# Optimization experiments

Measured on AMD Instinct MI355X. Metric: run time of the kernel, lower is better.

Reference implementation:

```python
import jax, jax.numpy as jnp
import numpy as np

B, N, D, H, HID = 8, 512, 512, 8, 2048


def setup_inputs() -> dict:
    key = jax.random.key(0)
    ks = jax.random.split(key, 8)
    s = 0.02
    p = lambda i, shape: jax.random.normal(ks[i], shape, jnp.float32) * s
    return dict(
        x=jax.random.normal(ks[0], (B, N, D), jnp.float32),
        Wq=p(1, (D, D)), bq=jnp.zeros((D,), jnp.float32),
        Wk=p(2, (D, D)), bk=jnp.zeros((D,), jnp.float32),
        Wv=p(3, (D, D)), bv=jnp.zeros((D,), jnp.float32),
        Wsig=p(4, (H, D)), bsig=jnp.zeros((H,), jnp.float32),
        ln1_g=jnp.ones((D,), jnp.float32), ln1_b=jnp.zeros((D,), jnp.float32),
        W1=p(5, (HID, D)), b1=jnp.zeros((HID,), jnp.float32),
        W2=p(6, (D, HID)), b2=jnp.zeros((D,), jnp.float32),
        ln2_g=jnp.ones((D,), jnp.float32), ln2_b=jnp.zeros((D,), jnp.float32),
    )


def _ln(z, g, b, eps=1e-5):
    m = jnp.mean(z, axis=-1, keepdims=True)
    v = jnp.var(z, axis=-1, keepdims=True)
    return (z - m) * jax.lax.rsqrt(v + eps) * g + b


def reference(x, Wq, bq, Wk, bk, Wv, bv, Wsig, bsig,
              ln1_g, ln1_b, W1, b1, W2, b2, ln2_g, ln2_b):
    Bb, Nn, Dd = x.shape
    Hh = bsig.shape[0]
    dh = Dd // Hh
    # --- AnomalyAttention: series attention S, Gaussian prior P, Z = S @ V ---
    Q = (x @ Wq.T + bq).reshape(Bb, Nn, Hh, dh)
    K = (x @ Wk.T + bk).reshape(Bb, Nn, Hh, dh)
    V = (x @ Wv.T + bv).reshape(Bb, Nn, Hh, dh)
    scores = jnp.einsum('bnhd,bmhd->bhnm', Q, K) / jnp.sqrt(jnp.float32(dh))
    S = jax.nn.softmax(scores, axis=-1)                       # [B,H,N,N]
    # learned positive scale sigma per (batch, position, head)
    sigma = jax.nn.softplus(x @ Wsig.T + bsig) + 1e-5         # [B,N,H]
    idx = jnp.arange(Nn, dtype=jnp.float32)
    dist2 = (idx[:, None] - idx[None, :]) ** 2                # [N,N]
    sig = jnp.transpose(sigma, (0, 2, 1))[..., None]          # [B,H,N,1]
    gauss = jnp.exp(-dist2 / (2.0 * sig * sig)) / (jnp.sqrt(2.0 * jnp.pi) * sig)
    P = gauss / jnp.sum(gauss, axis=-1, keepdims=True)        # row-normalized prior
    Zh = jnp.einsum('bhnm,bmhd->bnhd', S, V).reshape(Bb, Nn, Dd)
    # --- residual + LayerNorm + MLP(relu) + residual + LayerNorm ---
    Z = _ln(Zh + x, ln1_g, ln1_b)
    hidden = jax.nn.relu(Z @ W1.T + b1)
    x_hat = hidden @ W2.T + b2
    x_hat = _ln(x_hat + Z, ln2_g, ln2_b)
    return (x_hat, P, S)
```

## Files before the change

kernel.cpp:

```cpp
#include <hip/hip_runtime.h>
#include <cstdint>

typedef short s16x8 __attribute__((ext_vector_type(8)));
typedef float f32x4 __attribute__((ext_vector_type(4)));
using u16 = unsigned short;


__device__ __forceinline__ u16 f2bf(float f) {
    union { float f; uint32_t u; } v; v.f = f;
    uint32_t u = v.u;
    return (u16)((u + 0x7FFFu + ((u >> 16) & 1u)) >> 16);
}
__device__ __forceinline__ float bf2f(u16 u) {
    return __uint_as_float(((uint32_t)u) << 16);
}

__device__ __forceinline__ void gload_lds16(const void* g, void* l) {
    __builtin_amdgcn_global_load_lds(
        (const __attribute__((address_space(1))) unsigned int*)g,
        (__attribute__((address_space(3))) unsigned int*)l, 16, 0, 0);
}

__device__ __forceinline__ void prior_row(
    const float* __restrict__ sigT, float* __restrict__ P, int row, int lane)
{
    int n = row & 511;
    float s = sigT[row];
    float a = -1.0f / (2.0f * s * s);
    float e[8]; float sum = 0.f;
#pragma unroll
    for (int j = 0; j < 8; ++j) {
        float d = (float)(n - (lane * 8 + j));
        e[j] = __expf(a * d * d);
        sum += e[j];
    }
#pragma unroll
    for (int m = 1; m < 64; m <<= 1) sum += __shfl_xor(sum, m, 64);
    float r = 1.0f / sum;
    f32x4* dst = (f32x4*)(P + (long)row * 512 + lane * 8);
    dst[0] = (f32x4){e[0]*r, e[1]*r, e[2]*r, e[3]*r};
    dst[1] = (f32x4){e[4]*r, e[5]*r, e[6]*r, e[7]*r};
}

__global__ __launch_bounds__(256) void k_convert_sigma(
    const float* __restrict__ x, const float* __restrict__ wq,
    const float* __restrict__ wk, const float* __restrict__ wv,
    const float* __restrict__ w1, const float* __restrict__ w2,
    const float* __restrict__ bq, const float* __restrict__ bk,
    const float* __restrict__ bv,
    const float* __restrict__ Wsig, const float* __restrict__ bsig,
    u16* __restrict__ xb, u16* __restrict__ wqb, u16* __restrict__ wkb,
    u16* __restrict__ wvb, u16* __restrict__ w1b, u16* __restrict__ w2b,
    float* __restrict__ biascat, float* __restrict__ sigT)
{
    int bk_ = blockIdx.x;
    int tid = threadIdx.x;
    if (bk_ >= 4866) {
        int row  = (int)(((bk_ - 4866) * 256 + tid) >> 6);
        int lane = tid & 63;
        const float4* xr = (const float4*)(x + (long)row * 512);
        float4 xa = xr[lane * 2], xc = xr[lane * 2 + 1];
        float xs[8] = {xa.x, xa.y, xa.z, xa.w, xc.x, xc.y, xc.z, xc.w};
        float ph[8];
#pragma unroll
        for (int h = 0; h < 8; ++h) {
            const float4* wr = (const float4*)(Wsig + h * 512);
            float4 wa = wr[lane * 2], wc = wr[lane * 2 + 1];
            ph[h] = xs[0]*wa.x + xs[1]*wa.y + xs[2]*wa.z + xs[3]*wa.w
                  + xs[4]*wc.x + xs[5]*wc.y + xs[6]*wc.z + xs[7]*wc.w;
        }
#pragma unroll
        for (int h = 0; h < 8; ++h)
#pragma unroll
            for (int m = 1; m < 64; m <<= 1)
                ph[h] += __shfl_xor(ph[h], m, 64);
        if (lane < 8) {
            float z  = ph[lane] + bsig[lane];
            float sp = fmaxf(z, 0.f) + log1pf(__expf(-fabsf(z)));
            int b = row >> 9, n = row & 511;
            sigT[(((long)b * 8 + lane) << 9) + n] = sp + 1e-5f;
        }
        return;
    }
    long g = (long)bk_ * 256 + tid;
    if (g >= 1245184) {
        long id = g - 1245184;
        if (id < 384) {
            const float* src = id < 128 ? bq : id < 256 ? bk : bv;
            ((float4*)biascat)[id] = ((const float4*)src)[id & 127];
        }
        return;
    }
    const float* src; u16* dst; long off;
    if      (g <  524288) { src = x;  dst = xb;  off = g; }
    else if (g <  589824) { src = wq; dst = wqb; off = g -  524288; }
    else if (g <  655360) { src = wk; dst = wkb; off = g -  589824; }
    else if (g <  720896) { src = wv; dst = wvb; off = g -  655360; }
    else if (g <  983040) { src = w1; dst = w1b; off = g -  720896; }
    else                  { src = w2; dst = w2b; off = g -  983040; }
    float4 v = ((const float4*)src)[off];
    ushort4 o;
    o.x = f2bf(v.x); o.y = f2bf(v.y); o.z = f2bf(v.z); o.w = f2bf(v.w);
    ((ushort4*)dst)[off] = o;
}

template<int EPI>
__device__ __forceinline__ void gemm_epi(
    const float* __restrict__ bias, void* __restrict__ C,
    int gi, int gj, float v)
{
    if constexpr (EPI == 3) {
        v = fmaxf(v + bias[gj], 0.f);
        ((u16*)C)[(long)gi * 2048 + gj] = f2bf(v);
    } else if constexpr (EPI == 4) {
        ((float*)C)[(long)gi * 512 + gj] = v + bias[gj];
    } else {
        v += bias[gj];
        int mat = gj >> 9, cj = gj & 511;
        int h = cj >> 6, d = cj & 63, b = gi >> 9, n = gi & 511;
        u16* base = (u16*)C;
        if (mat == 0)
            base[(((long)(b * 8 + h) * 512 + n) << 6) + d] = f2bf(v);
        else if (mat == 1)
            (base + 2097152)[(((long)(b * 8 + h) * 512 + n) << 6) + d] = f2bf(v);
        else
            (base + 4194304)[(((long)(b * 8 + h) * 64 + d) << 9) + n] = f2bf(v);
    }
}

template<int BM, int BN, int EPI>
__device__ __forceinline__ void gemm_body(
    const u16* __restrict__ A, const u16* __restrict__ B,
    const float* __restrict__ bias, void* __restrict__ C,
    int lda, int ldb, int K, int bx, int by,
    u16* __restrict__ As, u16* __restrict__ Bs)
{
    constexpr int BK = 64;
    const u16* Ag = A + (long)bx * BM * lda;
    const u16* Bg = B + (long)by * BN * ldb;

    int tid  = threadIdx.x;
    int wave = tid >> 6, lane = tid & 63;
    int wm = wave >> 2, wn = wave & 3;
    constexpr int WTM = BM / 2, WTN = BN / 4;
    constexpr int FM = WTM / 16, FN = WTN / 16;
    int r16 = lane & 15, g4 = lane >> 4;

    f32x4 acc[FM][FN];
#pragma unroll
    for (int i = 0; i < FM; ++i)
#pragma unroll
        for (int j = 0; j < FN; ++j) acc[i][j] = (f32x4){0.f, 0.f, 0.f, 0.f};

    constexpr int nA = BM * BK / (512 * 8);
    constexpr int nB = BN * BK / (512 * 8);

    auto stage = [&](int buf, int k0) {
#pragma unroll
        for (int c = 0; c < nA; ++c) {
            int e = c * 512 + tid;
            int r = e >> 3, s = e & 7;
            gload_lds16(Ag + (long)r * lda + k0 + ((s ^ (r & 7)) * 8),
                        &As[buf * BM * BK + e * 8]);
        }
#pragma unroll
        for (int c = 0; c < nB; ++c) {
            int e = c * 512 + tid;
            int r = e >> 3, s = e & 7;
            gload_lds16(Bg + (long)r * ldb + k0 + ((s ^ (r & 7)) * 8),
                        &Bs[buf * BN * BK + e * 8]);
        }
    };

    stage(0, 0);
    __syncthreads();
    int cur = 0;
    const int NT = K / BK;
    for (int t = 0; t < NT; ++t) {
        if (t + 1 < NT) stage(cur ^ 1, (t + 1) * BK);
#pragma unroll
        for (int kk = 0; kk < 2; ++kk) {
            s16x8 af[FM], bfr[FN];
#pragma unroll
            for (int fm = 0; fm < FM; ++fm) {
                int row = wm * WTM + fm * 16 + r16;
                int slot = (kk * 4 + g4) ^ (row & 7);
                af[fm] = *(const s16x8*)&As[cur * BM * BK + row * 64 + slot * 8];
            }
#pragma unroll
            for (int fn = 0; fn < FN; ++fn) {
                int row = wn * WTN + fn * 16 + r16;
                int slot = (kk * 4 + g4) ^ (row & 7);
                bfr[fn] = *(const s16x8*)&Bs[cur * BN * BK + row * 64 + slot * 8];
            }
#pragma unroll
            for (int fm = 0; fm < FM; ++fm)
#pragma unroll
                for (int fn = 0; fn < FN; ++fn)
                    acc[fm][fn] = __builtin_amdgcn_mfma_f32_16x16x32_bf16(af[fm], bfr[fn], acc[fm][fn], 0, 0, 0);
        }
        __syncthreads();
        cur ^= 1;
    }

    int i0 = bx * BM + wm * WTM;
    int j0 = by * BN + wn * WTN;
#pragma unroll
    for (int fm = 0; fm < FM; ++fm)
#pragma unroll
        for (int fn = 0; fn < FN; ++fn)
#pragma unroll
            for (int j = 0; j < 4; ++j)
                gemm_epi<EPI>(bias, C,
                              i0 + fm * 16 + (g4 << 2) + j,
                              j0 + fn * 16 + r16, acc[fm][fn][j]);
}

template<int BM, int BN, int EPI>
__global__ __launch_bounds__(512) void k_gemm_nt(
    const u16* __restrict__ A, const u16* __restrict__ B,
    const float* __restrict__ bias, void* __restrict__ C,
    int lda, int ldb, int K)
{
    __shared__ __align__(16) u16 As[2 * BM * 64];
    __shared__ __align__(16) u16 Bs[2 * BN * 64];
    gemm_body<BM, BN, EPI>(A, B, bias, C, lda, ldb, K,
                           blockIdx.x, blockIdx.y, As, Bs);
}

__global__ __launch_bounds__(512) void k_qkv_prior(
    const u16* __restrict__ A, const u16* __restrict__ B,
    const float* __restrict__ bias, void* __restrict__ C,
    const float* __restrict__ sigT, float* __restrict__ P)
{
    __shared__ __align__(16) u16 As[2 * 128 * 64];
    __shared__ __align__(16) u16 Bs[2 * 128 * 64];
    int gid = blockIdx.x;
    if (gid < 384) {
        gemm_body<128, 128, 5>(A, B, bias, C, 512, 512, 512,
                               gid % 32, gid / 32, As, Bs);
        return;
    }
    int pid  = gid - 384;
    int wave = threadIdx.x >> 6, lane = threadIdx.x & 63;
    prior_row(sigT, P, 16384 + pid * 8 + wave, lane);
}

__global__ __launch_bounds__(256) void k_attn_prior(
    const u16* __restrict__ Qb, const u16* __restrict__ Kb,
    const u16* __restrict__ Vt, const float* __restrict__ sigT,
    float* __restrict__ S, float* __restrict__ Zh, float* __restrict__ P)
{
    __shared__ __align__(16) u16 Sb[4][16][264];
    __shared__ float cmbM[2][2][16];
    __shared__ float cmbS[2][2][16];
    __shared__ float zc[2][16][66];

    int gid = blockIdx.x;
    int tid = threadIdx.x;
    int wave = tid >> 6, lane = tid & 63;

    if (gid >= 1024) {
        prior_row(sigT, P, (gid - 1024) * 4 + wave, lane);
        return;
    }

    int bh = gid & 63;
    int rb = gid >> 6;
    int rg = wave >> 1, ch = wave & 1;
    int r16 = lane & 15, g4 = lane >> 4, hi8 = g4 * 8;

    int row0 = rb * 32 + rg * 16;
    const u16* Qg = Qb + ((long)bh * 512 + row0) * 64;
    const u16* Kg = Kb + ((long)bh * 512 + ch * 256) * 64;
    const u16* Vg = Vt + (long)bh * 64 * 512;

    s16x8 qa[2];
    qa[0] = *(const s16x8*)(Qg + r16 * 64 + hi8);
    qa[1] = *(const s16x8*)(Qg + r16 * 64 + 32 + hi8);

    f32x4 acc[16];
#pragma unroll
    for (int t = 0; t < 16; ++t) acc[t] = (f32x4){0.f, 0.f, 0.f, 0.f};

    __builtin_amdgcn_s_setprio(1);
#pragma unroll
    for (int kk = 0; kk < 2; ++kk)
#pragma unroll
        for (int t = 0; t < 16; ++t) {
            s16x8 b = *(const s16x8*)(Kg + (long)(t * 16 + r16) * 64 + kk * 32 + hi8);
            acc[t] = __builtin_amdgcn_mfma_f32_16x16x32_bf16(qa[kk], b, acc[t], 0, 0, 0);
        }
    __builtin_amdgcn_s_setprio(0);

    float mx[4] = {-1e30f, -1e30f, -1e30f, -1e30f};
#pragma unroll
    for (int t = 0; t < 16; ++t)
#pragma unroll
        for (int j = 0; j < 4; ++j) mx[j] = fmaxf(mx[j], acc[t][j]);
#pragma unroll
    for (int j = 0; j < 4; ++j)
#pragma unroll
        for (int m = 1; m < 16; m <<= 1) mx[j] = fmaxf(mx[j], __shfl_xor(mx[j], m, 64));

    float sm[4] = {0.f, 0.f, 0.f, 0.f};
#pragma unroll
    for (int t = 0; t < 16; ++t)
#pragma unroll
        for (int j = 0; j < 4; ++j) {
            float p = __expf(0.125f * (acc[t][j] - mx[j]));
            acc[t][j] = p;
            sm[j] += p;
        }
#pragma unroll
    for (int j = 0; j < 4; ++j)
#pragma unroll
        for (int m = 1; m < 16; m <<= 1) sm[j] += __shfl_xor(sm[j], m, 64);

    if (r16 == 0) {
#pragma unroll
        for (int j = 0; j < 4; ++j) {
            cmbM[rg][ch][g4 * 4 + j] = mx[j];
            cmbS[rg][ch][g4 * 4 + j] = sm[j];
        }
    }
    __syncthreads();

    float scale[4];
#pragma unroll
    for (int j = 0; j < 4; ++j) {
        float mo = cmbM[rg][ch ^ 1][g4 * 4 + j];
        float so = cmbS[rg][ch ^ 1][g4 * 4 + j];
        float M  = fmaxf(mx[j], mo);
        float tot = sm[j] * __expf(mx[j] - M) + so * __expf(mo - M);
        scale[j] = __expf(mx[j] - M) / tot;
    }
#pragma unroll
    for (int t = 0; t < 16; ++t)
#pragma unroll
        for (int j = 0; j < 4; ++j) acc[t][j] *= scale[j];

#pragma unroll
    for (int t = 0; t < 16; ++t)
#pragma unroll
        for (int j = 0; j < 4; ++j)
            Sb[wave][g4 * 4 + j][t * 16 + r16] = f2bf(acc[t][j]);

    long sbase = ((long)bh * 512 + row0) * 512 + ch * 256;
#pragma unroll
    for (int r = 0; r < 16; ++r) {
        ushort4 u = *(const ushort4*)&Sb[wave][r][lane * 4];
        *(f32x4*)&S[sbase + (long)r * 512 + lane * 4] =
            (f32x4){bf2f(u.x), bf2f(u.y), bf2f(u.z), bf2f(u.w)};
    }

    f32x4 zacc[4];
#pragma unroll
    for (int fn = 0; fn < 4; ++fn) zacc[fn] = (f32x4){0.f, 0.f, 0.f, 0.f};

    __builtin_amdgcn_s_setprio(1);
#pragma unroll
    for (int kb = 0; kb < 8; ++kb) {
        s16x8 pa = *(const s16x8*)&Sb[wave][r16][kb * 32 + hi8];
#pragma unroll
        for (int fn = 0; fn < 4; ++fn) {
            s16x8 vb = *(const s16x8*)(Vg + (long)(fn * 16 + r16) * 512 + ch * 256 + kb * 32 + hi8);
            zacc[fn] = __builtin_amdgcn_mfma_f32_16x16x32_bf16(pa, vb, zacc[fn], 0, 0, 0);
        }
    }
    __builtin_amdgcn_s_setprio(0);

    if (ch == 1) {
#pragma unroll
        for (int fn = 0; fn < 4; ++fn)
#pragma unroll
            for (int j = 0; j < 4; ++j)
                zc[rg][g4 * 4 + j][fn * 16 + r16] = zacc[fn][j];
    }
    __syncthreads();
    if (ch == 0) {
        long zb = ((long)(bh >> 3) * 512 + row0) * 512 + (bh & 7) * 64;
#pragma unroll
        for (int fn = 0; fn < 4; ++fn)
#pragma unroll
            for (int j = 0; j < 4; ++j)
                Zh[zb + (long)(g4 * 4 + j) * 512 + fn * 16 + r16] =
                    zacc[fn][j] + zc[rg][g4 * 4 + j][fn * 16 + r16];
    }
}

template<bool WBF>
__global__ __launch_bounds__(256) void k_ln(
    const float* __restrict__ a, const float* __restrict__ b,
    const float* __restrict__ g, const float* __restrict__ bt,
    float* __restrict__ y, u16* __restrict__ yb)
{
    int row  = (int)((blockIdx.x * 256 + threadIdx.x) >> 6);
    int lane = threadIdx.x & 63;
    const float4* ar = (const float4*)(a + (long)row * 512);
    const float4* br = (const float4*)(b + (long)row * 512);
    float4 a0 = ar[lane * 2], a1 = ar[lane * 2 + 1];
    float4 b0 = br[lane * 2], b1 = br[lane * 2 + 1];
    float v[8] = {a0.x + b0.x, a0.y + b0.y, a0.z + b0.z, a0.w + b0.w,
                  a1.x + b1.x, a1.y + b1.y, a1.z + b1.z, a1.w + b1.w};
    float s = 0.f, q = 0.f;
#pragma unroll
    for (int j = 0; j < 8; ++j) { s += v[j]; q += v[j] * v[j]; }
#pragma unroll
    for (int m = 1; m < 64; m <<= 1) {
        s += __shfl_xor(s, m, 64);
        q += __shfl_xor(q, m, 64);
    }
    float mean = s * (1.f / 512.f);
    float var  = q * (1.f / 512.f) - mean * mean;
    float rstd = rsqrtf(var + 1e-5f);
    const float4* gr = (const float4*)(g + lane * 8);
    const float4* tr = (const float4*)(bt + lane * 8);
    float4 g0 = gr[0], g1 = gr[1], t0 = tr[0], t1 = tr[1];
    float gg[8] = {g0.x, g0.y, g0.z, g0.w, g1.x, g1.y, g1.z, g1.w};
    float tt[8] = {t0.x, t0.y, t0.z, t0.w, t1.x, t1.y, t1.z, t1.w};
    float o[8];
#pragma unroll
    for (int j = 0; j < 8; ++j) o[j] = (v[j] - mean) * rstd * gg[j] + tt[j];
    float4* yr = (float4*)(y + (long)row * 512 + lane * 8);
    yr[0] = make_float4(o[0], o[1], o[2], o[3]);
    yr[1] = make_float4(o[4], o[5], o[6], o[7]);
    if constexpr (WBF) {
        s16x8 ob;
#pragma unroll
        for (int j = 0; j < 8; ++j) ob[j] = (short)f2bf(o[j]);
        *(s16x8*)(yb + (long)row * 512 + lane * 8) = ob;
    }
}

extern "C" void kernel_launch(void* const* d_in, const int* in_sizes, int n_in,
                              void* d_out, int out_size, void* d_ws, size_t ws_size,
                              hipStream_t stream)
{
    const float* x    = (const float*)d_in[0];
    const float* Wq   = (const float*)d_in[1];
    const float* bq   = (const float*)d_in[2];
    const float* Wk   = (const float*)d_in[3];
    const float* bk   = (const float*)d_in[4];
    const float* Wv   = (const float*)d_in[5];
    const float* bv   = (const float*)d_in[6];
    const float* Wsig = (const float*)d_in[7];
    const float* bsig = (const float*)d_in[8];
    const float* g1   = (const float*)d_in[9];
    const float* be1  = (const float*)d_in[10];
    const float* W1   = (const float*)d_in[11];
    const float* b1   = (const float*)d_in[12];
    const float* W2   = (const float*)d_in[13];
    const float* b2   = (const float*)d_in[14];
    const float* g2   = (const float*)d_in[15];
    const float* be2  = (const float*)d_in[16];

    float* out_xhat = (float*)d_out;
    float* out_P    = out_xhat + 2097152;
    float* out_S    = out_P + 16777216;

    char* ws = (char*)d_ws;
    u16*   xb   = (u16*)(ws + 0);
    u16*   Qb   = (u16*)(ws + 4194304);
    u16*   hid  = (u16*)(ws + 0);
    u16*   Wqb  = (u16*)(ws + 16777216);
    u16*   W1b  = (u16*)(ws + 18350080);
    u16*   W2b  = (u16*)(ws + 20447232);
    float* sigT = (float*)(ws + 22544384);
    float* Zh   = (float*)(ws + 22675456);
    float* bcat = (float*)(ws + 22675456);
    float* x2   = (float*)(ws + 22675456);
    float* Z    = (float*)(ws + 31064064);
    u16*   Zb   = (u16*)(ws + 39452672);

    u16* Wkb = Wqb + 262144;
    u16* Wvb = Wqb + 524288;

    k_convert_sigma<<<5890, 256, 0, stream>>>(x, Wq, Wk, Wv, W1, W2, bq, bk, bv,
                                              Wsig, bsig,
                                              xb, Wqb, Wkb, Wvb, W1b, W2b,
                                              bcat, sigT);

    k_qkv_prior<<<2432, 512, 0, stream>>>(xb, Wqb, bcat, Qb, sigT, out_P);

    k_attn_prior<<<5120, 256, 0, stream>>>(Qb, Qb + 2097152, Qb + 4194304,
                                           sigT, out_S, Zh, out_P);

    k_ln<true><<<1024,256,0,stream>>>(Zh, x, g1, be1, Z, Zb);

    k_gemm_nt<128,128,3><<<dim3(32,16,1),512,0,stream>>>(Zb, W1b, b1, hid, 512, 512, 512);

    k_gemm_nt<64,128,4><<<dim3(64,4,1),512,0,stream>>>(hid, W2b, b2, x2, 2048, 2048, 2048);

    k_ln<false><<<1024,256,0,stream>>>(x2, Z, g2, be2, out_xhat, nullptr);
}
```

Measured before the change: 133.8 us.

## Fuse both LayerNorms into producer kernels via last-block atomic counters

Removes the two standalone LayerNorm launches. Each attention block and each second-MLP GEMM tile bumps an atomic counter for its row group, and the last block to finish that group runs the residual add and LayerNorm over those rows. The counters are zeroed inside the existing conversion kernel. This saves two kernel launches and the gaps between them, but adds atomics, fences, and a serial LayerNorm tail on whichever block finishes last.

```diff
diff --git a/kernel.cpp b/kernel.cpp
--- a/kernel.cpp
+++ b/kernel.cpp
@@ -40,6 +40,48 @@
     f32x4* dst = (f32x4*)(P + (long)row * 512 + lane * 8);
     dst[0] = (f32x4){e[0]*r, e[1]*r, e[2]*r, e[3]*r};
     dst[1] = (f32x4){e[4]*r, e[5]*r, e[6]*r, e[7]*r};
+}
+
+template<bool WBF>
+__device__ __forceinline__ void ln_row(
+    const float* __restrict__ a, const float* __restrict__ b,
+    const float* __restrict__ g, const float* __restrict__ bt,
+    float* __restrict__ y, u16* __restrict__ yb, long row, int lane)
+{
+    const float4* ar = (const float4*)(a + row * 512);
+    const float4* br = (const float4*)(b + row * 512);
+    float4 a0 = ar[lane * 2], a1 = ar[lane * 2 + 1];
+    float4 b0 = br[lane * 2], b1 = br[lane * 2 + 1];
+    float v[8] = {a0.x + b0.x, a0.y + b0.y, a0.z + b0.z, a0.w + b0.w,
+                  a1.x + b1.x, a1.y + b1.y, a1.z + b1.z, a1.w + b1.w};
+    float s = 0.f, q = 0.f;
+#pragma unroll
+    for (int j = 0; j < 8; ++j) { s += v[j]; q += v[j] * v[j]; }
+#pragma unroll
+    for (int m = 1; m < 64; m <<= 1) {
+        s += __shfl_xor(s, m, 64);
+        q += __shfl_xor(q, m, 64);
+    }
+    float mean = s * (1.f / 512.f);
+    float var  = q * (1.f / 512.f) - mean * mean;
+    float rstd = rsqrtf(var + 1e-5f);
+    const float4* gr = (const float4*)(g + lane * 8);
+    const float4* tr = (const float4*)(bt + lane * 8);
+    float4 g0 = gr[0], g1 = gr[1], t0 = tr[0], t1 = tr[1];
+    float gg[8] = {g0.x, g0.y, g0.z, g0.w, g1.x, g1.y, g1.z, g1.w};
+    float tt[8] = {t0.x, t0.y, t0.z, t0.w, t1.x, t1.y, t1.z, t1.w};
+    float o[8];
+#pragma unroll
+    for (int j = 0; j < 8; ++j) o[j] = (v[j] - mean) * rstd * gg[j] + tt[j];
+    float4* yr = (float4*)(y + row * 512 + lane * 8);
+    yr[0] = make_float4(o[0], o[1], o[2], o[3]);
+    yr[1] = make_float4(o[4], o[5], o[6], o[7]);
+    if constexpr (WBF) {
+        s16x8 ob;
+#pragma unroll
+        for (int j = 0; j < 8; ++j) ob[j] = (short)f2bf(o[j]);
+        *(s16x8*)(yb + row * 512 + lane * 8) = ob;
+    }
 }
 
 __global__ __launch_bounds__(256) void k_convert_sigma(
@@ -51,7 +93,8 @@
     const float* __restrict__ Wsig, const float* __restrict__ bsig,
     u16* __restrict__ xb, u16* __restrict__ wqb, u16* __restrict__ wkb,
     u16* __restrict__ wvb, u16* __restrict__ w1b, u16* __restrict__ w2b,
-    float* __restrict__ biascat, float* __restrict__ sigT)
+    float* __restrict__ biascat, float* __restrict__ sigT,
+    int* __restrict__ cnt)
 {
     int bk_ = blockIdx.x;
     int tid = threadIdx.x;
@@ -88,6 +131,8 @@
         if (id < 384) {
             const float* src = id < 128 ? bq : id < 256 ? bk : bv;
             ((float4*)biascat)[id] = ((const float4*)src)[id & 127];
+        } else if (id < 432) {
+            ((int4*)cnt)[id - 384] = make_int4(0, 0, 0, 0);
         }
         return;
     }
@@ -246,15 +291,19 @@
     prior_row(sigT, P, 16384 + pid * 8 + wave, lane);
 }
 
-__global__ __launch_bounds__(256) void k_attn_prior(
+__global__ __launch_bounds__(256) void k_attn_prior_ln(
     const u16* __restrict__ Qb, const u16* __restrict__ Kb,
     const u16* __restrict__ Vt, const float* __restrict__ sigT,
-    float* __restrict__ S, float* __restrict__ Zh, float* __restrict__ P)
+    float* __restrict__ S, float* __restrict__ Zh, float* __restrict__ P,
+    const float* __restrict__ x, const float* __restrict__ g1,
+    const float* __restrict__ be1, float* __restrict__ Z,
+    u16* __restrict__ Zb, int* __restrict__ cnt)
 {
     __shared__ __align__(16) u16 Sb[4][16][264];
     __shared__ float cmbM[2][2][16];
     __shared__ float cmbS[2][2][16];
     __shared__ float zc[2][16][66];
+    __shared__ int lastf;
 
     int gid = blockIdx.x;
     int tid = threadIdx.x;
@@ -387,49 +436,56 @@
                 Zh[zb + (long)(g4 * 4 + j) * 512 + fn * 16 + r16] =
                     zacc[fn][j] + zc[rg][g4 * 4 + j][fn * 16 + r16];
     }
-}
-
-template<bool WBF>
-__global__ __launch_bounds__(256) void k_ln(
-    const float* __restrict__ a, const float* __restrict__ b,
-    const float* __restrict__ g, const float* __restrict__ bt,
-    float* __restrict__ y, u16* __restrict__ yb)
-{
-    int row  = (int)((blockIdx.x * 256 + threadIdx.x) >> 6);
-    int lane = threadIdx.x & 63;
-    const float4* ar = (const float4*)(a + (long)row * 512);
-    const float4* br = (const float4*)(b + (long)row * 512);
-    float4 a0 = ar[lane * 2], a1 = ar[lane * 2 + 1];
-    float4 b0 = br[lane * 2], b1 = br[lane * 2 + 1];
-    float v[8] = {a0.x + b0.x, a0.y + b0.y, a0.z + b0.z, a0.w + b0.w,
-                  a1.x + b1.x, a1.y + b1.y, a1.z + b1.z, a1.w + b1.w};
-    float s = 0.f, q = 0.f;
-#pragma unroll
-    for (int j = 0; j < 8; ++j) { s += v[j]; q += v[j] * v[j]; }
-#pragma unroll
-    for (int m = 1; m < 64; m <<= 1) {
-        s += __shfl_xor(s, m, 64);
-        q += __shfl_xor(q, m, 64);
-    }
-    float mean = s * (1.f / 512.f);
-    float var  = q * (1.f / 512.f) - mean * mean;
-    float rstd = rsqrtf(var + 1e-5f);
-    const float4* gr = (const float4*)(g + lane * 8);
-    const float4* tr = (const float4*)(bt + lane * 8);
-    float4 g0 = gr[0], g1 = gr[1], t0 = tr[0], t1 = tr[1];
-    float gg[8] = {g0.x, g0.y, g0.z, g0.w, g1.x, g1.y, g1.z, g1.w};
-    float tt[8] = {t0.x, t0.y, t0.z, t0.w, t1.x, t1.y, t1.z, t1.w};
-    float o[8];
-#pragma unroll
-    for (int j = 0; j < 8; ++j) o[j] = (v[j] - mean) * rstd * gg[j] + tt[j];
-    float4* yr = (float4*)(y + (long)row * 512 + lane * 8);
-    yr[0] = make_float4(o[0], o[1], o[2], o[3]);
-    yr[1] = make_float4(o[4], o[5], o[6], o[7]);
-    if constexpr (WBF) {
-        s16x8 ob;
-#pragma unroll
-        for (int j = 0; j < 8; ++j) ob[j] = (short)f2bf(o[j]);
-        *(s16x8*)(yb + (long)row * 512 + lane * 8) = ob;
+
+    __syncthreads();
+    if (tid == 0) {
+        int old = __hip_atomic_fetch_add(&cnt[(bh >> 3) * 16 + rb], 1,
+                                         __ATOMIC_ACQ_REL,
+                                         __HIP_MEMORY_SCOPE_AGENT);
+        lastf = (old == 7);
+    }
+    __syncthreads();
+    if (lastf) {
+        __threadfence();
+        long rbase = (long)(bh >> 3) * 512 + rb * 32;
+#pragma unroll
+        for (int rr = 0; rr < 8; ++rr)
+            ln_row<true>(Zh, x, g1, be1, Z, Zb,
+                         rbase + wave * 8 + rr, lane);
+    }
+}
+
+__global__ __launch_bounds__(512) void k_mlp2_ln(
+    const u16* __restrict__ A, const u16* __restrict__ B,
+    const float* __restrict__ bias, float* __restrict__ x2,
+    const float* __restrict__ Z, const float* __restrict__ g2,
+    const float* __restrict__ be2, float* __restrict__ xhat,
+    int* __restrict__ cnt)
+{
+    __shared__ __align__(16) u16 As[2 * 64 * 64];
+    __shared__ __align__(16) u16 Bs[2 * 128 * 64];
+    __shared__ int lastf;
+
+    int bx = blockIdx.x, by = blockIdx.y;
+    gemm_body<64, 128, 4>(A, B, bias, x2, 2048, 2048, 2048, bx, by, As, Bs);
+
+    int tid = threadIdx.x;
+    int wave = tid >> 6, lane = tid & 63;
+
+    __syncthreads();
+    if (tid == 0) {
+        int old = __hip_atomic_fetch_add(&cnt[bx], 1, __ATOMIC_ACQ_REL,
+                                         __HIP_MEMORY_SCOPE_AGENT);
+        lastf = (old == 3);
+    }
+    __syncthreads();
+    if (lastf) {
+        __threadfence();
+        long rbase = (long)bx * 64;
+#pragma unroll
+        for (int rr = 0; rr < 8; ++rr)
+            ln_row<false>(x2, Z, g2, be2, xhat, nullptr,
+                          rbase + wave * 8 + rr, lane);
     }
 }
 
@@ -472,6 +528,7 @@
     float* x2   = (float*)(ws + 22675456);
     float* Z    = (float*)(ws + 31064064);
     u16*   Zb   = (u16*)(ws + 39452672);
+    int*   cnt  = (int*)(ws + 43646976);
 
     u16* Wkb = Wqb + 262144;
     u16* Wvb = Wqb + 524288;
@@ -479,18 +536,16 @@
     k_convert_sigma<<<5890, 256, 0, stream>>>(x, Wq, Wk, Wv, W1, W2, bq, bk, bv,
                                               Wsig, bsig,
                                               xb, Wqb, Wkb, Wvb, W1b, W2b,
-                                              bcat, sigT);
+                                              bcat, sigT, cnt);
 
     k_qkv_prior<<<2432, 512, 0, stream>>>(xb, Wqb, bcat, Qb, sigT, out_P);
 
-    k_attn_prior<<<5120, 256, 0, stream>>>(Qb, Qb + 2097152, Qb + 4194304,
-                                           sigT, out_S, Zh, out_P);
-
-    k_ln<true><<<1024,256,0,stream>>>(Zh, x, g1, be1, Z, Zb);
+    k_attn_prior_ln<<<5120, 256, 0, stream>>>(Qb, Qb + 2097152, Qb + 4194304,
+                                              sigT, out_S, Zh, out_P,
+                                              x, g1, be1, Z, Zb, cnt);
 
     k_gemm_nt<128,128,3><<<dim3(32,16,1),512,0,stream>>>(Zb, W1b, b1, hid, 512, 512, 512);
 
-    k_gemm_nt<64,128,4><<<dim3(64,4,1),512,0,stream>>>(hid, W2b, b2, x2, 2048, 2048, 2048);
-
-    k_ln<false><<<1024,256,0,stream>>>(x2, Z, g2, be2, out_xhat, nullptr);
-}
+    k_mlp2_ln<<<dim3(64,4,1),512,0,stream>>>(hid, W2b, b2, x2, Z, g2, be2,
+                                             out_xhat, cnt + 128);
+}
```

New measurement: 274.2 us. +105.0%, slower.
